# Kernel tuning notes

Hardware: AMD Instinct MI355X
Metric: run time of the kernel (lower is better)

## Reference

```python
import jax, jax.numpy as jnp
import numpy as np

# HRR ops (holoformer): bind = circular convolution via FFT; unbind = circular
# correlation (bind with the approximate inverse), i.e. conj in freq domain.

def _fft(a):
    return jnp.fft.fft(a, axis=-1)

def _bind_f(Fa, Fb):
    return jnp.fft.ifft(Fa * Fb, axis=-1).real

def _unbind_f(Fs, Fk):
    return jnp.fft.ifft(Fs * jnp.conj(Fk), axis=-1).real


def setup_inputs() -> dict:
    key = jax.random.key(0)
    B, S, D = 4, 4096, 1024
    ks = jax.random.split(key, 5)
    scale = 1.0 / np.sqrt(D)
    inp = {
        "x": jax.random.normal(ks[0], (B, S, D), dtype=jnp.float32),
        "Wq": jax.random.normal(ks[1], (D, D), dtype=jnp.float32) * scale,
        "bq": jnp.zeros((D,), jnp.float32),
        "Wk": jax.random.normal(ks[2], (D, D), dtype=jnp.float32) * scale,
        "bk": jnp.zeros((D,), jnp.float32),
        "Wv": jax.random.normal(ks[3], (D, D), dtype=jnp.float32) * scale,
        "bv": jnp.zeros((D,), jnp.float32),
        "Wr": jax.random.normal(ks[4], (D, D), dtype=jnp.float32) * scale,
        "br": jnp.zeros((D,), jnp.float32),
    }
    return inp


def reference(x, Wq, bq, Wk, bk, Wv, bv, Wr, br):
    # tanh-gated linear projections (nn.Linear stores weight as [out, in])
    query = jnp.tanh(jnp.einsum('bsd,ed->bse', x, Wq) + bq)
    keys = jnp.tanh(jnp.einsum('bsd,ed->bse', x, Wk) + bk)
    values = jnp.tanh(jnp.einsum('bsd,ed->bse', x, Wv) + bv)
    remove_query = jnp.tanh(jnp.einsum('bsd,ed->bse', x, Wr) + br)

    # bind(keys, values) and sum over sequence -> s: (B, 1, D)
    x_k = _bind_f(_fft(keys), _fft(values))
    s = x_k.sum(axis=1, keepdims=True)
    Fs = _fft(s)

    # retrieve with query, add
    retrieved = _unbind_f(Fs, _fft(query))
    out = x + retrieved

    # remove: bind(remove_query, unbind(s, remove_query))
    Fr = _fft(remove_query)
    remove_values = _unbind_f(Fs, Fr)
    removes = _bind_f(Fr, _fft(remove_values))
    out = out - removes
    return out
```

## Files before the change

### kernel.cpp

```cpp
#include <hip/hip_runtime.h>
#include <hip/hip_fp16.h>

#define D 1024
#define LOG2D 10
#define S_LEN 4096
#define BATCH 4
#define NROWS (BATCH * S_LEN)
#define PI_F 3.14159265358979323846f

#define SLOT(p) ((p) + ((p) >> 4))
#define FBUF 1088
#define NTW 341

typedef _Float16 f16x8 __attribute__((ext_vector_type(8)));
typedef float f32x4 __attribute__((ext_vector_type(4)));

__device__ __forceinline__ float2 cmul(float2 a, float2 b) {
    return make_float2(a.x * b.x - a.y * b.y, a.x * b.y + a.y * b.x);
}

__device__ __forceinline__ float fast_tanh(float v) {
    float e = __expf(2.0f * v);
    return 1.0f - 2.0f * __builtin_amdgcn_rcpf(e + 1.0f);
}

__device__ __forceinline__ void g2lds16(const void* g, void* l) {
    __builtin_amdgcn_global_load_lds(
        (const __attribute__((address_space(1))) unsigned int*)g,
        (__attribute__((address_space(3))) unsigned int*)l, 16, 0, 0);
}

__global__ __launch_bounds__(256) void convert_all(
    const float* __restrict__ x,
    const float* __restrict__ w0, const float* __restrict__ w1,
    const float* __restrict__ w2, const float* __restrict__ w3,
    __half* __restrict__ xh,
    __half* __restrict__ h0, __half* __restrict__ h1,
    __half* __restrict__ h2, __half* __restrict__ h3)
{
    const int b = blockIdx.x;
    const float* s;
    __half* d;
    int li;
    if (b < 16384) { s = x; d = xh; li = b; }
    else {
        int t = b - 16384;
        int r = t >> 10;
        li = t & 1023;
        s = (r == 0) ? w0 : (r == 1) ? w1 : (r == 2) ? w2 : w3;
        d = (r == 0) ? h0 : (r == 1) ? h1 : (r == 2) ? h2 : h3;
    }
    const int idx = li * 256 + threadIdx.x;
    float4 v = ((const float4*)s)[idx];
    __half2 lo = __floats2half2_rn(v.x, v.y);
    __half2 hi = __floats2half2_rn(v.z, v.w);
    ((__half2*)d)[2 * idx + 0] = lo;
    ((__half2*)d)[2 * idx + 1] = hi;
}

__global__ __launch_bounds__(256, 2) void gemm_mfma2(
    const __half* __restrict__ Xh,
    const __half* __restrict__ W0, const float* __restrict__ b0, __half* __restrict__ O0,
    const __half* __restrict__ W1, const float* __restrict__ b1, __half* __restrict__ O1)
{
    const int idx = blockIdx.x;
    const int xcd = idx & 7;
    const int j = idx >> 3;
    const int n0 = (j & 7) * 128;
    const int m0 = (xcd * 16 + (j >> 3)) * 128;

    __shared__ __align__(16) __half As[2][128 * 32];
    __shared__ __align__(16) __half B0s[2][128 * 32];
    __shared__ __align__(16) __half B1s[2][128 * 32];

    const int tid = threadIdx.x;
    const int wave = tid >> 6;
    const int lane = tid & 63;

    const int srow = lane >> 2;
    const int schunk = (lane & 3) ^ ((lane >> 3) & 3);

    const __half* gA[2];
    const __half* gB0[2];
    const __half* gB1[2];
    int loff[2];
#pragma unroll
    for (int c = 0; c < 2; ++c) {
        const int rg = (wave * 2 + c) * 16 + srow;
        gA[c]  = Xh + (size_t)(m0 + rg) * 1024 + schunk * 8;
        gB0[c] = W0 + (size_t)(n0 + rg) * 1024 + schunk * 8;
        gB1[c] = W1 + (size_t)(n0 + rg) * 1024 + schunk * 8;
        loff[c] = (wave * 2 + c) * 512;
    }

    const int wm = (wave & 1) * 64;
    const int wn = (wave >> 1) * 64;
    const int quad = lane >> 4;
    const int l15 = lane & 15;

    int aoff[4], boff[4];
#pragma unroll
    for (int i = 0; i < 4; ++i) {
        const int Ra = wm + i * 16 + l15;
        aoff[i] = Ra * 32 + (quad ^ ((Ra >> 1) & 3)) * 8;
        const int Rb = wn + i * 16 + l15;
        boff[i] = Rb * 32 + (quad ^ ((Rb >> 1) & 3)) * 8;
    }

    f32x4 acc0[4][4], acc1[4][4];
#pragma unroll
    for (int i = 0; i < 4; ++i)
#pragma unroll
        for (int jj = 0; jj < 4; ++jj) {
            acc0[i][jj] = (f32x4){0.f, 0.f, 0.f, 0.f};
            acc1[i][jj] = (f32x4){0.f, 0.f, 0.f, 0.f};
        }

#pragma unroll
    for (int c = 0; c < 2; ++c) {
        g2lds16(gA[c],  &As[0][loff[c]]);
        g2lds16(gB0[c], &B0s[0][loff[c]]);
        g2lds16(gB1[c], &B1s[0][loff[c]]);
    }

    for (int kt = 0; kt < 32; ++kt) {
        const int cur = kt & 1;
        __syncthreads();
        if (kt < 31) {
            const int kh = (kt + 1) * 32;
            const int nxt = cur ^ 1;
#pragma unroll
            for (int c = 0; c < 2; ++c) {
                g2lds16(gA[c] + kh,  &As[nxt][loff[c]]);
                g2lds16(gB0[c] + kh, &B0s[nxt][loff[c]]);
                g2lds16(gB1[c] + kh, &B1s[nxt][loff[c]]);
            }
        }

        f16x8 af[4], bf0[4], bf1[4];
#pragma unroll
        for (int i = 0; i < 4; ++i) af[i] = *(const f16x8*)(&As[cur][0] + aoff[i]);
#pragma unroll
        for (int jj = 0; jj < 4; ++jj) {
            bf0[jj] = *(const f16x8*)(&B0s[cur][0] + boff[jj]);
            bf1[jj] = *(const f16x8*)(&B1s[cur][0] + boff[jj]);
        }
#pragma unroll
        for (int i = 0; i < 4; ++i)
#pragma unroll
            for (int jj = 0; jj < 4; ++jj) {
                acc0[i][jj] = __builtin_amdgcn_mfma_f32_16x16x32_f16(af[i], bf0[jj], acc0[i][jj], 0, 0, 0);
                acc1[i][jj] = __builtin_amdgcn_mfma_f32_16x16x32_f16(af[i], bf1[jj], acc1[i][jj], 0, 0, 0);
            }
    }

#pragma unroll
    for (int jj = 0; jj < 4; ++jj) {
        const int n = n0 + wn + jj * 16 + l15;
        const float bv0 = b0[n];
        const float bv1 = b1[n];
#pragma unroll
        for (int i = 0; i < 4; ++i) {
            const int mbase = m0 + wm + i * 16 + quad * 4;
#pragma unroll
            for (int r = 0; r < 4; ++r) {
                O0[(size_t)(mbase + r) * 1024 + n] = __float2half(fast_tanh(acc0[i][jj][r] + bv0));
                O1[(size_t)(mbase + r) * 1024 + n] = __float2half(fast_tanh(acc1[i][jj][r] + bv1));
            }
        }
    }
}

__device__ __forceinline__ void build_twiddles_r4(float2* Wts, int tid) {
    for (int j = tid; j < NTW; j += 256) {
        int k, m;
        if (j == 0)      { k = 0;      m = 1;   }
        else if (j < 5)  { k = j - 1;  m = 4;   }
        else if (j < 21) { k = j - 5;  m = 16;  }
        else if (j < 85) { k = j - 21; m = 64;  }
        else             { k = j - 85; m = 256; }
        float ang = PI_F * (float)k / (2.0f * (float)m);
        Wts[j] = make_float2(cosf(ang), -sinf(ang));
    }
}

__device__ void fft1024_r4(float2* bufA, float2* bufB, const float2* Wts,
                           float dir, int tid) {
    float2* src = bufA;
    float2* dst = bufB;
    int m = 1;
#pragma unroll
    for (int s = 0; s < 5; ++s) {
        __syncthreads();
        const int k = tid & (m - 1);
        const int jb = tid >> (2 * s);
        float2 x0 = src[SLOT(tid)];
        float2 x1 = src[SLOT(tid + 256)];
        float2 x2 = src[SLOT(tid + 512)];
        float2 x3 = src[SLOT(tid + 768)];
        float2 y1, y2, y3;
        if (s == 0) { y1 = x1; y2 = x2; y3 = x3; }
        else {
            const int soff = (m - 1) / 3;
            float2 t1 = Wts[soff + k];
            t1.y *= dir;
            float2 t2 = cmul(t1, t1);
            float2 t3 = cmul(t1, t2);
            y1 = cmul(x1, t1);
            y2 = cmul(x2, t2);
            y3 = cmul(x3, t3);
        }
        float2 a = make_float2(x0.x + y2.x, x0.y + y2.y);
        float2 b = make_float2(x0.x - y2.x, x0.y - y2.y);
        float2 c = make_float2(y1.x + y3.x, y1.y + y3.y);
        float2 d = make_float2(y1.x - y3.x, y1.y - y3.y);
        float2 e = make_float2(dir * d.y, -dir * d.x);
        const int o = (jb << (2 * s + 2)) + k;
        dst[SLOT(o)]         = make_float2(a.x + c.x, a.y + c.y);
        dst[SLOT(o + m)]     = make_float2(b.x + e.x, b.y + e.y);
        dst[SLOT(o + 2 * m)] = make_float2(a.x - c.x, a.y - c.y);
        dst[SLOT(o + 3 * m)] = make_float2(b.x - e.x, b.y - e.y);
        float2* t = src; src = dst; dst = t;
        m <<= 2;
    }
    __syncthreads();
}

#define ROWS_PER_BLOCK 8
__global__ __launch_bounds__(256) void bind_accum_kernel(
    const __half* __restrict__ K, const __half* __restrict__ V, float2* __restrict__ Fs)
{
    __shared__ __align__(16) float2 bufA[FBUF];
    __shared__ __align__(16) float2 bufB[FBUF];
    __shared__ __align__(16) float2 Wts[NTW];
    const int tid = threadIdx.x;
    build_twiddles_r4(Wts, tid);

    const int row0 = blockIdx.x * ROWS_PER_BLOCK;
    const int b = row0 >> 12;

    float2 accr[4];
#pragma unroll
    for (int h = 0; h < 4; ++h) accr[h] = make_float2(0.f, 0.f);

    for (int r = 0; r < ROWS_PER_BLOCK; ++r) {
        const size_t base = (size_t)(row0 + r) * D;
#pragma unroll
        for (int h = 0; h < 4; ++h) {
            const int j = tid + (h << 8);
            bufA[SLOT(j)] = make_float2(__half2float(K[base + j]), __half2float(V[base + j]));
        }
        fft1024_r4(bufA, bufB, Wts, 1.0f, tid);
#pragma unroll
        for (int h = 0; h < 4; ++h) {
            const int j = tid + (h << 8);
            const int j2 = (D - j) & (D - 1);
            float2 Zt = bufB[SLOT(j)];
            float2 Zc = bufB[SLOT(j2)]; Zc.y = -Zc.y;
            float2 Fk = make_float2(0.5f * (Zt.x + Zc.x), 0.5f * (Zt.y + Zc.y));
            float2 Fv = make_float2(0.5f * (Zt.y - Zc.y), -0.5f * (Zt.x - Zc.x));
            float2 P = cmul(Fk, Fv);
            accr[h].x += P.x; accr[h].y += P.y;
        }
    }
#pragma unroll
    for (int h = 0; h < 4; ++h) {
        const int j = tid + (h << 8);
        atomicAdd(&Fs[(size_t)b * D + j].x, accr[h].x);
        atomicAdd(&Fs[(size_t)b * D + j].y, accr[h].y);
    }
}

__global__ __launch_bounds__(256) void retrieve_kernel(
    const __half* __restrict__ Q, const __half* __restrict__ R,
    const float2* __restrict__ Fs, const float* __restrict__ x, float* __restrict__ out)
{
    __shared__ __align__(16) float2 bufA[FBUF];
    __shared__ __align__(16) float2 bufB[FBUF];
    __shared__ __align__(16) float2 Wts[NTW];
    const int tid = threadIdx.x;
    build_twiddles_r4(Wts, tid);

    const int row = blockIdx.x;
    const int b = row >> 12;
    const size_t base = (size_t)row * D;

#pragma unroll
    for (int h = 0; h < 4; ++h) {
        const int j = tid + (h << 8);
        bufA[SLOT(j)] = make_float2(__half2float(Q[base + j]), __half2float(R[base + j]));
    }
    fft1024_r4(bufA, bufB, Wts, 1.0f, tid);

#pragma unroll
    for (int h = 0; h < 4; ++h) {
        const int j = tid + (h << 8);
        const int j2 = (D - j) & (D - 1);
        float2 Zt = bufB[SLOT(j)];
        float2 Zc = bufB[SLOT(j2)]; Zc.y = -Zc.y;
        float2 Fq = make_float2(0.5f * (Zt.x + Zc.x), 0.5f * (Zt.y + Zc.y));
        float2 Fr = make_float2(0.5f * (Zt.y - Zc.y), -0.5f * (Zt.x - Zc.x));
        float2 g  = make_float2(Fq.x - (Fr.x * Fr.x + Fr.y * Fr.y), -Fq.y);
        float2 Ff = Fs[(size_t)b * D + j];
        bufA[SLOT(j)] = cmul(Ff, g);
    }
    fft1024_r4(bufA, bufB, Wts, -1.0f, tid);

    const float inv = 1.0f / (float)D;
#pragma unroll
    for (int h = 0; h < 4; ++h) {
        const int j = tid + (h << 8);
        out[base + j] = x[base + j] + bufB[SLOT(j)].x * inv;
    }
}

extern "C" void kernel_launch(void* const* d_in, const int* in_sizes, int n_in,
                              void* d_out, int out_size, void* d_ws, size_t ws_size,
                              hipStream_t stream) {
    const float* x  = (const float*)d_in[0];
    const float* Wq = (const float*)d_in[1];
    const float* bq = (const float*)d_in[2];
    const float* Wk = (const float*)d_in[3];
    const float* bk = (const float*)d_in[4];
    const float* Wv = (const float*)d_in[5];
    const float* bv = (const float*)d_in[6];
    const float* Wr = (const float*)d_in[7];
    const float* br = (const float*)d_in[8];
    float* out = (float*)d_out;

    __half* P0 = (__half*)d_ws;
    __half* P1 = (__half*)((char*)d_ws + (size_t)NROWS * D * 2);
    float2* Fs = (float2*)((char*)d_ws + (size_t)NROWS * D * 4);

    __half* Xh  = (__half*)d_out;
    __half* Whk = (__half*)d_out + (size_t)16 * 1024 * 1024;
    __half* Whv = Whk + (size_t)1024 * 1024;
    __half* Whq = Whv + (size_t)1024 * 1024;
    __half* Whr = Whq + (size_t)1024 * 1024;

    convert_all<<<16384 + 4 * 1024, 256, 0, stream>>>(
        x, Wk, Wv, Wq, Wr, Xh, Whk, Whv, Whq, Whr);

    hipMemsetAsync(Fs, 0, (size_t)BATCH * D * sizeof(float2), stream);

    gemm_mfma2<<<1024, 256, 0, stream>>>(Xh, Whk, bk, P0, Whv, bv, P1);
    bind_accum_kernel<<<NROWS / ROWS_PER_BLOCK, 256, 0, stream>>>(P0, P1, Fs);
    gemm_mfma2<<<1024, 256, 0, stream>>>(Xh, Whq, bq, P0, Whr, br, P1);
    retrieve_kernel<<<NROWS, 256, 0, stream>>>(P0, P1, Fs, x, out);
}
```

Baseline: 498.7 us.

## Use single-buffered BK=64 LDS tiles with new XOR swizzle in dual GEMM

Switches the fused two-output GEMM from double-buffered K=32 LDS tiles to single-buffered K=64 tiles. This halves the number of K iterations and changes the row/chunk XOR swizzle to fit the 64-wide rows. It gives up the prefetch overlap: loads are now issued and waited on with two barriers per iteration, so global latency is no longer hidden behind MFMA work. LDS footprint stays the same.

```diff
diff --git a/kernel.cpp b/kernel.cpp
--- a/kernel.cpp
+++ b/kernel.cpp
@@ -69,28 +69,28 @@
     const int n0 = (j & 7) * 128;
     const int m0 = (xcd * 16 + (j >> 3)) * 128;
 
-    __shared__ __align__(16) __half As[2][128 * 32];
-    __shared__ __align__(16) __half B0s[2][128 * 32];
-    __shared__ __align__(16) __half B1s[2][128 * 32];
+    __shared__ __align__(16) __half As[128 * 64];
+    __shared__ __align__(16) __half B0s[128 * 64];
+    __shared__ __align__(16) __half B1s[128 * 64];
 
     const int tid = threadIdx.x;
     const int wave = tid >> 6;
     const int lane = tid & 63;
 
-    const int srow = lane >> 2;
-    const int schunk = (lane & 3) ^ ((lane >> 3) & 3);
-
-    const __half* gA[2];
-    const __half* gB0[2];
-    const __half* gB1[2];
-    int loff[2];
-#pragma unroll
-    for (int c = 0; c < 2; ++c) {
-        const int rg = (wave * 2 + c) * 16 + srow;
-        gA[c]  = Xh + (size_t)(m0 + rg) * 1024 + schunk * 8;
-        gB0[c] = W0 + (size_t)(n0 + rg) * 1024 + schunk * 8;
-        gB1[c] = W1 + (size_t)(n0 + rg) * 1024 + schunk * 8;
-        loff[c] = (wave * 2 + c) * 512;
+    const int srow = lane >> 3;
+    const int schunk = (lane & 7) ^ (lane >> 3);
+
+    const __half* gA[4];
+    const __half* gB0[4];
+    const __half* gB1[4];
+    int loff[4];
+#pragma unroll
+    for (int c = 0; c < 4; ++c) {
+        const int rbase = wave * 32 + c * 8;
+        gA[c]  = Xh + (size_t)(m0 + rbase + srow) * 1024 + schunk * 8;
+        gB0[c] = W0 + (size_t)(n0 + rbase + srow) * 1024 + schunk * 8;
+        gB1[c] = W1 + (size_t)(n0 + rbase + srow) * 1024 + schunk * 8;
+        loff[c] = rbase * 64;
     }
 
     const int wm = (wave & 1) * 64;
@@ -98,14 +98,16 @@
     const int quad = lane >> 4;
     const int l15 = lane & 15;
 
-    int aoff[4], boff[4];
-#pragma unroll
-    for (int i = 0; i < 4; ++i) {
-        const int Ra = wm + i * 16 + l15;
-        aoff[i] = Ra * 32 + (quad ^ ((Ra >> 1) & 3)) * 8;
-        const int Rb = wn + i * 16 + l15;
-        boff[i] = Rb * 32 + (quad ^ ((Rb >> 1) & 3)) * 8;
-    }
+    int aoff[2][4], boff[2][4];
+#pragma unroll
+    for (int kk = 0; kk < 2; ++kk)
+#pragma unroll
+        for (int i = 0; i < 4; ++i) {
+            const int Ra = wm + i * 16 + l15;
+            aoff[kk][i] = Ra * 64 + ((((kk << 2) | quad)) ^ (l15 & 7)) * 8;
+            const int Rb = wn + i * 16 + l15;
+            boff[kk][i] = Rb * 64 + ((((kk << 2) | quad)) ^ (l15 & 7)) * 8;
+        }
 
     f32x4 acc0[4][4], acc1[4][4];
 #pragma unroll
@@ -116,42 +118,35 @@
             acc1[i][jj] = (f32x4){0.f, 0.f, 0.f, 0.f};
         }
 
-#pragma unroll
-    for (int c = 0; c < 2; ++c) {
-        g2lds16(gA[c],  &As[0][loff[c]]);
-        g2lds16(gB0[c], &B0s[0][loff[c]]);
-        g2lds16(gB1[c], &B1s[0][loff[c]]);
-    }
-
-    for (int kt = 0; kt < 32; ++kt) {
-        const int cur = kt & 1;
+    for (int kt = 0; kt < 16; ++kt) {
+        const int kh = kt * 64;
         __syncthreads();
-        if (kt < 31) {
-            const int kh = (kt + 1) * 32;
-            const int nxt = cur ^ 1;
-#pragma unroll
-            for (int c = 0; c < 2; ++c) {
-                g2lds16(gA[c] + kh,  &As[nxt][loff[c]]);
-                g2lds16(gB0[c] + kh, &B0s[nxt][loff[c]]);
-                g2lds16(gB1[c] + kh, &B1s[nxt][loff[c]]);
+#pragma unroll
+        for (int c = 0; c < 4; ++c) {
+            g2lds16(gA[c] + kh,  As  + loff[c]);
+            g2lds16(gB0[c] + kh, B0s + loff[c]);
+            g2lds16(gB1[c] + kh, B1s + loff[c]);
+        }
+        __syncthreads();
+
+#pragma unroll
+        for (int kk = 0; kk < 2; ++kk) {
+            f16x8 af[4], bf0[4], bf1[4];
+#pragma unroll
+            for (int i = 0; i < 4; ++i) af[i] = *(const f16x8*)(As + aoff[kk][i]);
+#pragma unroll
+            for (int jj = 0; jj < 4; ++jj) {
+                bf0[jj] = *(const f16x8*)(B0s + boff[kk][jj]);
+                bf1[jj] = *(const f16x8*)(B1s + boff[kk][jj]);
             }
-        }
-
-        f16x8 af[4], bf0[4], bf1[4];
-#pragma unroll
-        for (int i = 0; i < 4; ++i) af[i] = *(const f16x8*)(&As[cur][0] + aoff[i]);
-#pragma unroll
-        for (int jj = 0; jj < 4; ++jj) {
-            bf0[jj] = *(const f16x8*)(&B0s[cur][0] + boff[jj]);
-            bf1[jj] = *(const f16x8*)(&B1s[cur][0] + boff[jj]);
-        }
-#pragma unroll
-        for (int i = 0; i < 4; ++i)
-#pragma unroll
-            for (int jj = 0; jj < 4; ++jj) {
-                acc0[i][jj] = __builtin_amdgcn_mfma_f32_16x16x32_f16(af[i], bf0[jj], acc0[i][jj], 0, 0, 0);
-                acc1[i][jj] = __builtin_amdgcn_mfma_f32_16x16x32_f16(af[i], bf1[jj], acc1[i][jj], 0, 0, 0);
-            }
+#pragma unroll
+            for (int i = 0; i < 4; ++i)
+#pragma unroll
+                for (int jj = 0; jj < 4; ++jj) {
+                    acc0[i][jj] = __builtin_amdgcn_mfma_f32_16x16x32_f16(af[i], bf0[jj], acc0[i][jj], 0, 0, 0);
+                    acc1[i][jj] = __builtin_amdgcn_mfma_f32_16x16x32_f16(af[i], bf1[jj], acc1[i][jj], 0, 0, 0);
+                }
+        }
     }
 
 #pragma unroll
```

After: 467.7 us. -6.2%, faster.
